# Kernel optimization log

Hardware: AMD Instinct MI355X
Metric: run time of the kernel (lower is better)

## Reference

```python
import jax, jax.numpy as jnp
import numpy as np

INPUT_SIZE = 512
HIDDEN_SIZE = 2048
OUTPUT_SIZE = 512
NUM_LAYERS = 4
INNER = INPUT_SIZE + HIDDEN_SIZE  # 2560
BATCH = 4096


def setup_inputs() -> dict:
    key = jax.random.key(0)
    ks = jax.random.split(key, 5)
    scale = 1.0 / np.sqrt(INNER)  # kaiming-uniform-like scale for nn.Linear
    x = jax.random.normal(ks[0], (BATCH, INPUT_SIZE), dtype=jnp.float32)
    h = jax.random.normal(ks[1], (BATCH, HIDDEN_SIZE), dtype=jnp.float32)
    W_layers = jax.random.normal(ks[2], (NUM_LAYERS, INNER, INNER), dtype=jnp.float32) * scale
    b_layers = jnp.zeros((NUM_LAYERS, INNER), dtype=jnp.float32)
    W_i2h = jax.random.normal(ks[3], (HIDDEN_SIZE, INNER), dtype=jnp.float32) * scale
    b_i2h = jnp.zeros((HIDDEN_SIZE,), dtype=jnp.float32)
    W_i2o = jax.random.normal(ks[4], (OUTPUT_SIZE, INNER), dtype=jnp.float32) * scale
    b_i2o = jnp.zeros((OUTPUT_SIZE,), dtype=jnp.float32)
    return {"x": x, "h": h, "W_layers": W_layers, "b_layers": b_layers,
            "W_i2h": W_i2h, "b_i2h": b_i2h, "W_i2o": W_i2o, "b_i2o": b_i2o}


def reference(x, h, W_layers, b_layers, W_i2h, b_i2h, W_i2o, b_i2o):
    # combined: [B, inner]
    combined = jnp.concatenate([x, h], axis=1)
    # stack of square Hebbian linear layers + ReLU (imprint trace writes are
    # state side effects only; they do not affect the forward output)
    for l in range(W_layers.shape[0]):
        combined = jax.nn.relu(jnp.einsum('bi,oi->bo', combined, W_layers[l]) + b_layers[l])
    hidden = jnp.tanh(jnp.einsum('bi,oi->bo', combined, W_i2h) + b_i2h)
    output = jnp.einsum('bi,oi->bo', combined, W_i2o) + b_i2o
    return (output, hidden)
```

## Files before the change

kernel.cpp:

```cpp
#include <hip/hip_runtime.h>
#include <hip/hip_bf16.h>

#define BATCH 4096
#define IN_SZ 512
#define HID_SZ 2048
#define OUT_SZ 512
#define NLAYER 4
#define INNER 2560
#define NKT (INNER / 64)


typedef __attribute__((ext_vector_type(8))) short bf16x8;
typedef __attribute__((ext_vector_type(4))) float f32x4;

__device__ __forceinline__ unsigned short f2bf(float f) {
  unsigned int u = __float_as_uint(f);
  u += 0x7fff + ((u >> 16) & 1);
  return (unsigned short)(u >> 16);
}

__device__ __forceinline__ void gload16(const void* g, void* l) {
  __builtin_amdgcn_global_load_lds(
      (const __attribute__((address_space(1))) unsigned int*)g,
      (__attribute__((address_space(3))) unsigned int*)l,
      16, 0, 0);
}


#define NWL4  6553600
#define NWO4  327680
#define NWH4  1310720
__global__ void cvt_all(const float* __restrict__ Wl, const float* __restrict__ Wih,
                        const float* __restrict__ Wio, unsigned short* __restrict__ dst) {
  const int n4 = NWL4 + NWO4 + NWH4;
  int i = blockIdx.x * blockDim.x + threadIdx.x;
  const int stride = gridDim.x * blockDim.x;
  for (; i < n4; i += stride) {
    const float* src;
    long off4;
    if (i < NWL4) { src = Wl; off4 = i; }
    else if (i < NWL4 + NWO4) { src = Wio; off4 = i - NWL4; }
    else { src = Wih; off4 = i - NWL4 - NWO4; }
    float4 v = *reinterpret_cast<const float4*>(src + off4 * 4);
    ushort4 o;
    o.x = f2bf(v.x); o.y = f2bf(v.y); o.z = f2bf(v.z); o.w = f2bf(v.w);
    *reinterpret_cast<ushort4*>(dst + (long)i * 4) = o;
  }
}

__global__ void build_combined(const float* __restrict__ x,
                               const float* __restrict__ h,
                               unsigned short* __restrict__ out) {
  const int n4 = BATCH * INNER / 4;
  int i = blockIdx.x * blockDim.x + threadIdx.x;
  const int stride = gridDim.x * blockDim.x;
  for (; i < n4; i += stride) {
    int row = i / (INNER / 4);
    int c4 = i - row * (INNER / 4);
    const float* src = (c4 < IN_SZ / 4) ? (x + (long)row * IN_SZ + c4 * 4)
                                        : (h + (long)row * HID_SZ + (c4 - IN_SZ / 4) * 4);
    float4 v = *reinterpret_cast<const float4*>(src);
    ushort4 o;
    o.x = f2bf(v.x); o.y = f2bf(v.y); o.z = f2bf(v.z); o.w = f2bf(v.w);
    *reinterpret_cast<ushort4*>(out + (long)i * 4) = o;
  }
}


#define STAGE_U(kt, u, buf) do {                                              \
  if ((u) < 4) {                                                              \
    const int base_ = (u) * 32 + w * 8;                                       \
    gload16(A + (long)(row0 + base_ + srow) * INNER + (kt) * 64 + srcsw,      \
            (void*)(&lds[buf][base_ * 64]));                                  \
  } else {                                                                    \
    const int base_ = ((u) - 4) * 32 + w * 8;                                 \
    gload16(B + (long)(col0 + base_ + srow) * INNER + (kt) * 64 + srcsw,      \
            (void*)(&lds[buf][8192 + base_ * 64]));                           \
  } } while (0)

#define LOAD_AF(dst, mh, buf) do {                                           \
  const unsigned short* Ar_ = &lds[buf][0];                                  \
  _Pragma("unroll")                                                          \
  for (int m_ = 0; m_ < 2; ++m_) {                                           \
    int r_ = wr * 64 + (mh) * 32 + m_ * 16 + fr;                             \
    dst[m_][0] = *(const bf16x8*)(Ar_ + r_ * 64 + csw0);                     \
    dst[m_][1] = *(const bf16x8*)(Ar_ + r_ * 64 + csw1);                     \
  } } while (0)

#define LOAD_BQA(dst, buf) do {                                              \
  const unsigned short* Br_ = &lds[buf][8192];                               \
  _Pragma("unroll")                                                          \
  for (int n_ = 0; n_ < 3; ++n_) {                                           \
    int r_ = wcn * 80 + n_ * 16 + fr;                                        \
    dst[n_][0] = *(const bf16x8*)(Br_ + r_ * 64 + csw0);                     \
    dst[n_][1] = *(const bf16x8*)(Br_ + r_ * 64 + csw1);                     \
  } } while (0)

#define LOAD_BQB(dst, buf) do {                                              \
  const unsigned short* Br_ = &lds[buf][8192];                               \
  _Pragma("unroll")                                                          \
  for (int n_ = 0; n_ < 2; ++n_) {                                           \
    int r_ = wcn * 80 + (3 + n_) * 16 + fr;                                  \
    dst[n_][0] = *(const bf16x8*)(Br_ + r_ * 64 + csw0);                     \
    dst[n_][1] = *(const bf16x8*)(Br_ + r_ * 64 + csw1);                     \
  } } while (0)

#define MF_A(af, bq, mh) do {                                                 \
  __builtin_amdgcn_s_setprio(1);                                              \
  _Pragma("unroll")                                                           \
  for (int m_ = 0; m_ < 2; ++m_)                                              \
    _Pragma("unroll")                                                         \
    for (int n_ = 0; n_ < 3; ++n_) {                                          \
      acc[(mh) * 2 + m_][n_] = __builtin_amdgcn_mfma_f32_16x16x32_bf16(       \
          af[m_][0], bq[n_][0], acc[(mh) * 2 + m_][n_], 0, 0, 0);             \
      acc[(mh) * 2 + m_][n_] = __builtin_amdgcn_mfma_f32_16x16x32_bf16(       \
          af[m_][1], bq[n_][1], acc[(mh) * 2 + m_][n_], 0, 0, 0);             \
    }                                                                         \
  __builtin_amdgcn_s_setprio(0);                                              \
} while (0)

#define MF_B(af, bq, mh) do {                                                 \
  __builtin_amdgcn_s_setprio(1);                                              \
  _Pragma("unroll")                                                           \
  for (int m_ = 0; m_ < 2; ++m_)                                              \
    _Pragma("unroll")                                                         \
    for (int n_ = 0; n_ < 2; ++n_) {                                          \
      acc[(mh) * 2 + m_][3 + n_] = __builtin_amdgcn_mfma_f32_16x16x32_bf16(   \
          af[m_][0], bq[n_][0], acc[(mh) * 2 + m_][3 + n_], 0, 0, 0);         \
      acc[(mh) * 2 + m_][3 + n_] = __builtin_amdgcn_mfma_f32_16x16x32_bf16(   \
          af[m_][1], bq[n_][1], acc[(mh) * 2 + m_][3 + n_], 0, 0, 0);         \
    }                                                                         \
  __builtin_amdgcn_s_setprio(0);                                              \
} while (0)

#define SB() __builtin_amdgcn_sched_barrier(0)

#define TILE_BODY(d, AC, QC, AN, QN) do {                                     \
  const int T = T2 + (d);                                                     \
  const int kt1 = (T + 1 < NKT) ? T + 1 : NKT - 1;    \
  const int kt2 = (T + 2 < NKT) ? T + 2 : NKT - 1;                            \
        \
  LOAD_BQB(bqB, d);                                                           \
  STAGE_U(kt1, 6, (d) ^ 1); STAGE_U(kt1, 7, (d) ^ 1); STAGE_U(kt1, 8, (d) ^ 1); \
  SB();                                                                       \
  asm volatile("s_waitcnt lgkmcnt(4)" ::: "memory");          \
  SB();                                                                       \
  MF_A(AC, QC, 0);                                                            \
          \
  LOAD_AF(afB, 1, d);                                                         \
  STAGE_U(kt1, 0, (d) ^ 1); STAGE_U(kt1, 1, (d) ^ 1);                         \
  SB();                                                                       \
  asm volatile("s_waitcnt lgkmcnt(4)" ::: "memory");            \
  SB();                                                                       \
  MF_B(AC, bqB, 0);                                                           \
  __builtin_amdgcn_s_barrier();   \
           \
  STAGE_U(kt2, 4, d); STAGE_U(kt2, 5, d);                                     \
  SB();                                                                       \
  asm volatile("s_waitcnt lgkmcnt(0)" ::: "memory");            \
  SB();                                                                       \
  MF_B(afB, bqB, 1);                                                          \
  __builtin_amdgcn_s_barrier();     \
       \
  STAGE_U(kt2, 2, d); STAGE_U(kt2, 3, d);                                     \
  asm volatile("s_waitcnt vmcnt(4)" ::: "memory");      \
  __builtin_amdgcn_s_barrier();            \
  SB();                                                                       \
  LOAD_AF(AN, 0, (d) ^ 1);                                                    \
  LOAD_BQA(QN, (d) ^ 1);                                                      \
  SB();                           \
  MF_A(afB, QC, 1);                                                           \
} while (0)

template <int MODE>
__global__ __launch_bounds__(256, 2)
void gemm8(const unsigned short* __restrict__ A, const unsigned short* __restrict__ B,
           const float* __restrict__ bias0, const float* __restrict__ bias1,
           void* __restrict__ C) {
  __shared__ unsigned short lds[2][18432];

  const int tid = threadIdx.x;
  const int w = tid >> 6;
  const int lane = tid & 63;

  const int flat = blockIdx.x;
  const int xcd = flat & 7;
  const int local = flat >> 3;
  const int nb = xcd * 2 + (local & 1);
  const int mb = local >> 1;
  const int row0 = mb * 128, col0 = nb * 160;
  const int wr = w >> 1, wcn = w & 1;

  const int srow = lane >> 3;
  const int srcsw = ((((lane & 7) << 4) ^ ((lane >> 3) << 4)) >> 1);

  const int fr = lane & 15;
  const int csw0 = ((((lane >> 4) << 4)) ^ ((lane & 7) << 4)) >> 1;
  const int csw1 = ((64 + ((lane >> 4) << 4)) ^ ((lane & 7) << 4)) >> 1;

  f32x4 acc[4][5] = {};
  bf16x8 afA0[2][2], afA1[2][2], afB[2][2];
  bf16x8 bqA0[3][2], bqA1[3][2], bqB[2][2];

  STAGE_U(0, 0, 0); STAGE_U(0, 1, 0); STAGE_U(0, 2, 0); STAGE_U(0, 3, 0);
  STAGE_U(0, 4, 0); STAGE_U(0, 5, 0); STAGE_U(0, 6, 0); STAGE_U(0, 7, 0);
  STAGE_U(0, 8, 0);
  STAGE_U(1, 4, 1); STAGE_U(1, 5, 1); STAGE_U(1, 2, 1); STAGE_U(1, 3, 1);
  asm volatile("s_waitcnt vmcnt(4)" ::: "memory");
  __builtin_amdgcn_s_barrier();
  SB();
  LOAD_AF(afA0, 0, 0);
  LOAD_BQA(bqA0, 0);
  SB();

  for (int T2 = 0; T2 < NKT; T2 += 2) {
    TILE_BODY(0, afA0, bqA0, afA1, bqA1);
    TILE_BODY(1, afA1, bqA1, afA0, bqA0);
  }
  asm volatile("s_waitcnt vmcnt(0)" ::: "memory");

  const int erow = row0 + wr * 64 + ((lane >> 4) << 2);
  const int ecol = col0 + wcn * 80 + fr;
  if (MODE == 0) {
    unsigned short* Co = (unsigned short*)C;
#pragma unroll
    for (int n = 0; n < 5; ++n) {
      const int col = ecol + n * 16;
      const float bv = bias0[col];
#pragma unroll
      for (int m = 0; m < 4; ++m) {
        const int row = erow + m * 16;
#pragma unroll
        for (int j = 0; j < 4; ++j) {
          float v = acc[m][n][j] + bv;
          v = fmaxf(v, 0.0f);
          Co[(long)(row + j) * INNER + col] = f2bf(v);
        }
      }
    }
  } else {
    float* outO = (float*)C;
    float* outH = (float*)C + (long)BATCH * OUT_SZ;
#pragma unroll
    for (int n = 0; n < 5; ++n) {
      const int col = ecol + n * 16;
      if (col < OUT_SZ) {
        const float bv = bias0[col];
#pragma unroll
        for (int m = 0; m < 4; ++m) {
          const int row = erow + m * 16;
#pragma unroll
          for (int j = 0; j < 4; ++j)
            outO[(long)(row + j) * OUT_SZ + col] = acc[m][n][j] + bv;
        }
      } else {
        const int hc = col - OUT_SZ;
        const float bv = bias1[hc];
#pragma unroll
        for (int m = 0; m < 4; ++m) {
          const int row = erow + m * 16;
#pragma unroll
          for (int j = 0; j < 4; ++j)
            outH[(long)(row + j) * HID_SZ + hc] = tanhf(acc[m][n][j] + bv);
        }
      }
    }
  }
}


extern "C" void kernel_launch(void* const* d_in, const int* in_sizes, int n_in,
                              void* d_out, int out_size, void* d_ws, size_t ws_size,
                              hipStream_t stream) {
  const float* x   = (const float*)d_in[0];
  const float* h   = (const float*)d_in[1];
  const float* Wl  = (const float*)d_in[2];
  const float* bl  = (const float*)d_in[3];
  const float* Wih = (const float*)d_in[4];
  const float* bih = (const float*)d_in[5];
  const float* Wio = (const float*)d_in[6];
  const float* bio = (const float*)d_in[7];

  unsigned short* ws   = (unsigned short*)d_ws;
  unsigned short* Wlb  = ws;
  unsigned short* Whb  = Wlb + (long)NLAYER * INNER * INNER;
  unsigned short* act0 = Whb + (long)INNER * INNER;
  unsigned short* act1 = act0 + (long)BATCH * INNER;

  cvt_all<<<2048, 256, 0, stream>>>(Wl, Wih, Wio, Wlb);
  build_combined<<<2048, 256, 0, stream>>>(x, h, act0);

  unsigned short* a_in = act0;
  unsigned short* a_out = act1;
  for (int l = 0; l < NLAYER; ++l) {
    gemm8<0><<<512, 256, 0, stream>>>(a_in, Wlb + (long)l * INNER * INNER,
                                      bl + (long)l * INNER, nullptr, a_out);
    unsigned short* t = a_in; a_in = a_out; a_out = t;
  }

  gemm8<1><<<512, 256, 0, stream>>>(a_in, Whb, bio, bih, d_out);
}
```

Measured before the change: 300.5 us.

## Overlap next-layer weight conversion with GEMM using an extra producer wave

Only layer 0's weights and the combined input are converted to bf16 up front, now in one merged prep kernel. The fp32-to-bf16 conversion of the next layer's weights (and of the i2o/i2h weights during the last layer) moves into a fifth wave in each GEMM block. That wave streams the conversion and takes part in the same number of block barriers as the compute waves. This hides most of the standalone conversion pass behind the compute-bound GEMMs. The cost is extra memory traffic during the GEMM, a tighter register budget from the 320-thread launch bounds (possible spills), and a fixed barrier count that must match the compute loop exactly.

```diff
diff --git a/kernel.cpp b/kernel.cpp
--- a/kernel.cpp
+++ b/kernel.cpp
@@ -26,43 +26,32 @@
       16, 0, 0);
 }
 
-
-#define NWL4  6553600
-#define NWO4  327680
-#define NWH4  1310720
-__global__ void cvt_all(const float* __restrict__ Wl, const float* __restrict__ Wih,
-                        const float* __restrict__ Wio, unsigned short* __restrict__ dst) {
-  const int n4 = NWL4 + NWO4 + NWH4;
+#define NW14 1638400
+#define NC4  2621440
+__global__ void prep(const float* __restrict__ W0, const float* __restrict__ x,
+                     const float* __restrict__ h, unsigned short* __restrict__ Wdst,
+                     unsigned short* __restrict__ cdst) {
+  const int total = NW14 + NC4;
   int i = blockIdx.x * blockDim.x + threadIdx.x;
   const int stride = gridDim.x * blockDim.x;
-  for (; i < n4; i += stride) {
+  for (; i < total; i += stride) {
     const float* src;
-    long off4;
-    if (i < NWL4) { src = Wl; off4 = i; }
-    else if (i < NWL4 + NWO4) { src = Wio; off4 = i - NWL4; }
-    else { src = Wih; off4 = i - NWL4 - NWO4; }
-    float4 v = *reinterpret_cast<const float4*>(src + off4 * 4);
-    ushort4 o;
-    o.x = f2bf(v.x); o.y = f2bf(v.y); o.z = f2bf(v.z); o.w = f2bf(v.w);
-    *reinterpret_cast<ushort4*>(dst + (long)i * 4) = o;
-  }
-}
-
-__global__ void build_combined(const float* __restrict__ x,
-                               const float* __restrict__ h,
-                               unsigned short* __restrict__ out) {
-  const int n4 = BATCH * INNER / 4;
-  int i = blockIdx.x * blockDim.x + threadIdx.x;
-  const int stride = gridDim.x * blockDim.x;
-  for (; i < n4; i += stride) {
-    int row = i / (INNER / 4);
-    int c4 = i - row * (INNER / 4);
-    const float* src = (c4 < IN_SZ / 4) ? (x + (long)row * IN_SZ + c4 * 4)
-                                        : (h + (long)row * HID_SZ + (c4 - IN_SZ / 4) * 4);
+    unsigned short* dst;
+    if (i < NW14) {
+      src = W0 + (long)i * 4;
+      dst = Wdst + (long)i * 4;
+    } else {
+      const int j = i - NW14;
+      const int row = j / (INNER / 4);
+      const int c4 = j - row * (INNER / 4);
+      src = (c4 < IN_SZ / 4) ? (x + (long)row * IN_SZ + c4 * 4)
+                             : (h + (long)row * HID_SZ + (c4 - IN_SZ / 4) * 4);
+      dst = cdst + (long)j * 4;
+    }
     float4 v = *reinterpret_cast<const float4*>(src);
     ushort4 o;
     o.x = f2bf(v.x); o.y = f2bf(v.y); o.z = f2bf(v.z); o.w = f2bf(v.w);
-    *reinterpret_cast<ushort4*>(out + (long)i * 4) = o;
+    *reinterpret_cast<ushort4*>(dst) = o;
   }
 }
 
@@ -153,14 +142,14 @@
   asm volatile("s_waitcnt lgkmcnt(4)" ::: "memory");            \
   SB();                                                                       \
   MF_B(AC, bqB, 0);                                                           \
-  __builtin_amdgcn_s_barrier();   \
+  __builtin_amdgcn_s_barrier();            \
            \
   STAGE_U(kt2, 4, d); STAGE_U(kt2, 5, d);                                     \
   SB();                                                                       \
   asm volatile("s_waitcnt lgkmcnt(0)" ::: "memory");            \
   SB();                                                                       \
   MF_B(afB, bqB, 1);                                                          \
-  __builtin_amdgcn_s_barrier();     \
+  __builtin_amdgcn_s_barrier();                 \
        \
   STAGE_U(kt2, 2, d); STAGE_U(kt2, 3, d);                                     \
   asm volatile("s_waitcnt vmcnt(4)" ::: "memory");      \
@@ -173,17 +162,69 @@
 } while (0)
 
 template <int MODE>
-__global__ __launch_bounds__(256, 2)
+__global__ __launch_bounds__(320, 2)
 void gemm8(const unsigned short* __restrict__ A, const unsigned short* __restrict__ B,
            const float* __restrict__ bias0, const float* __restrict__ bias1,
-           void* __restrict__ C) {
+           void* __restrict__ C,
+           const float* __restrict__ cvtA, const float* __restrict__ cvtB,
+           int csplit, int cnk, unsigned short* __restrict__ cvtD) {
   __shared__ unsigned short lds[2][18432];
 
   const int tid = threadIdx.x;
   const int w = tid >> 6;
   const int lane = tid & 63;
-
   const int flat = blockIdx.x;
+
+  if (w == 4) {
+    const long base = (long)flat * 64 + lane;
+    const long stride = 32768;
+    int k = 0;
+    float4 p0, p1;
+    long u0 = 0, u1 = 0;
+    bool have = false;
+    for (int s = 0; s < 121; ++s) {
+      if (have) {
+        ushort4 o0, o1;
+        o0.x = f2bf(p0.x); o0.y = f2bf(p0.y); o0.z = f2bf(p0.z); o0.w = f2bf(p0.w);
+        o1.x = f2bf(p1.x); o1.y = f2bf(p1.y); o1.z = f2bf(p1.z); o1.w = f2bf(p1.w);
+        *reinterpret_cast<ushort4*>(cvtD + u0 * 4) = o0;
+        *reinterpret_cast<ushort4*>(cvtD + u1 * 4) = o1;
+        have = false;
+      }
+      if (k < cnk) {
+        u0 = base + (long)k * stride;
+        u1 = base + (long)(k + 1) * stride;
+        {
+          const long e = u0 * 4;
+          const int row = (int)(e / INNER);
+          const int col = (int)(e - (long)row * INNER);
+          const float* sp = (row < csplit) ? (cvtA + (long)row * INNER + col)
+                                           : (cvtB + (long)(row - csplit) * INNER + col);
+          p0 = *reinterpret_cast<const float4*>(sp);
+        }
+        {
+          const long e = u1 * 4;
+          const int row = (int)(e / INNER);
+          const int col = (int)(e - (long)row * INNER);
+          const float* sp = (row < csplit) ? (cvtA + (long)row * INNER + col)
+                                           : (cvtB + (long)(row - csplit) * INNER + col);
+          p1 = *reinterpret_cast<const float4*>(sp);
+        }
+        k += 2;
+        have = true;
+      }
+      __builtin_amdgcn_s_barrier();
+    }
+    if (have) {
+      ushort4 o0, o1;
+      o0.x = f2bf(p0.x); o0.y = f2bf(p0.y); o0.z = f2bf(p0.z); o0.w = f2bf(p0.w);
+      o1.x = f2bf(p1.x); o1.y = f2bf(p1.y); o1.z = f2bf(p1.z); o1.w = f2bf(p1.w);
+      *reinterpret_cast<ushort4*>(cvtD + u0 * 4) = o0;
+      *reinterpret_cast<ushort4*>(cvtD + u1 * 4) = o1;
+    }
+    return;
+  }
+
   const int xcd = flat & 7;
   const int local = flat >> 3;
   const int nb = xcd * 2 + (local & 1);
@@ -287,16 +328,26 @@
   unsigned short* act0 = Whb + (long)INNER * INNER;
   unsigned short* act1 = act0 + (long)BATCH * INNER;
 
-  cvt_all<<<2048, 256, 0, stream>>>(Wl, Wih, Wio, Wlb);
-  build_combined<<<2048, 256, 0, stream>>>(x, h, act0);
+  const long WSZ = (long)INNER * INNER;
+  const int BIG = 1 << 30;
+
+  prep<<<2048, 256, 0, stream>>>(Wl, x, h, Wlb, act0);
 
   unsigned short* a_in = act0;
   unsigned short* a_out = act1;
   for (int l = 0; l < NLAYER; ++l) {
-    gemm8<0><<<512, 256, 0, stream>>>(a_in, Wlb + (long)l * INNER * INNER,
-                                      bl + (long)l * INNER, nullptr, a_out);
+    const float* cA; const float* cB; int split; unsigned short* cD;
+    if (l < NLAYER - 1) {
+      cA = Wl + (l + 1) * WSZ; cB = cA; split = BIG; cD = Wlb + (l + 1) * WSZ;
+    } else {
+      cA = Wio; cB = Wih; split = OUT_SZ; cD = Whb;
+    }
+    gemm8<0><<<512, 320, 0, stream>>>(a_in, Wlb + (long)l * WSZ,
+                                      bl + (long)l * INNER, nullptr, a_out,
+                                      cA, cB, split, 50, cD);
     unsigned short* t = a_in; a_in = a_out; a_out = t;
   }
 
-  gemm8<1><<<512, 256, 0, stream>>>(a_in, Whb, bio, bih, d_out);
-}
+  gemm8<1><<<512, 320, 0, stream>>>(a_in, Whb, bio, bih, d_out,
+                                    Wl, Wl, BIG, 0, Wlb);
+}
```

Measured after the change: 445.8 us. 1.48x slower.
